# Optimization experiments

Measured on AMD Instinct MI355X. Metric: run time of the kernel, lower is better.

## Reference

```python
import jax, jax.numpy as jnp
import numpy as np

ALPHA = 0.2  # LeakyReLU negative slope


def _gat_layer(h, dst, adj, w, a_in, a_out, b):
    # h: [N, F_in], dst: [N, K] int (edge (i,k): i -> dst[i,k]), adj: [N, K]
    hid = h @ w                      # [N, D]
    s_in = hid @ a_in                # [N]  (attention applied to source-node half)
    s_out = hid @ a_out              # [N]  (attention applied to dest-node half)
    # edge scores, grouped per source node (matches view(-1, num_neighs) softmax)
    e = jax.nn.leaky_relu(s_in[:, None] + s_out[dst], ALPHA)   # [N, K]
    # torch code detaches attention (Variable(..., requires_grad=False))
    att = jax.lax.stop_gradient(jax.nn.softmax(e, axis=1))     # [N, K]
    w_edge = adj * att                                          # [N, K]
    # SpMM: out[i] = sum_k w_edge[i,k] * hid[dst[i,k]]
    out = jnp.einsum('nk,nkd->nd', w_edge, hid[dst]) + b        # [N, D]
    return out


def setup_inputs() -> dict:
    key = jax.random.key(0)
    ks = jax.random.split(key, 12)
    N, K, F, H, O = 100000, 16, 128, 128, 128
    stdv1 = 1.0 / np.sqrt(H)
    stdv2 = 1.0 / np.sqrt(O)
    u = lambda k, shp, s: jax.random.uniform(k, shp, jnp.float32, -s, s)
    return {
        'x': jax.random.normal(ks[0], (N, F), jnp.float32),
        'dst_idx': jax.random.randint(ks[1], (N, K), 0, N),
        'adj_vals': jax.random.uniform(ks[2], (N, K), jnp.float32),
        'w1': u(ks[3], (F, H), stdv1),
        'a_in1': jax.random.normal(ks[4], (H,), jnp.float32) * (1.414 / np.sqrt(H)),
        'a_out1': jax.random.normal(ks[5], (H,), jnp.float32) * (1.414 / np.sqrt(H)),
        'b1': u(ks[6], (H,), stdv1),
        'w2': u(ks[7], (H, O), stdv2),
        'a_in2': jax.random.normal(ks[8], (O,), jnp.float32) * (1.414 / np.sqrt(O)),
        'a_out2': jax.random.normal(ks[9], (O,), jnp.float32) * (1.414 / np.sqrt(O)),
        'b2': u(ks[10], (O,), stdv2),
    }


def reference(x, dst_idx, adj_vals, w1, a_in1, a_out1, b1, w2, a_in2, a_out2, b2):
    h = jax.nn.relu(_gat_layer(x, dst_idx, adj_vals, w1, a_in1, a_out1, b1))
    h = jax.nn.relu(_gat_layer(h, dst_idx, adj_vals, w2, a_in2, a_out2, b2))
    return h
```

## Files before the change

kernel.cpp:

```cpp
#include <hip/hip_runtime.h>

#define ALPHA 0.2f
#define LDA 136

typedef short bf16x8 __attribute__((ext_vector_type(8)));
typedef float f32x4  __attribute__((ext_vector_type(4)));

static __device__ __forceinline__ float bf2f(unsigned short u) {
    union { unsigned int i; float f; } v; v.i = ((unsigned int)u) << 16; return v.f;
}
static __device__ __forceinline__ unsigned short f2bf(float f) {
    union { float f; unsigned int i; } v; v.f = f;
    unsigned int x = v.i;
    return (unsigned short)((x + 0x7fffu + ((x >> 16) & 1u)) >> 16);
}

__global__ __launch_bounds__(128)
void prep_wT_kernel(const float* __restrict__ w1, const float* __restrict__ w2,
                    unsigned short* __restrict__ wT1, unsigned short* __restrict__ wT2)
{
    const int b = blockIdx.x;
    const float* w = (b >> 4) ? w2 : w1;
    unsigned short* wT = (b >> 4) ? wT2 : wT1;
    const int k0 = (b & 15) * 8;
    const int c = threadIdx.x;

    ushort4 u0, u1;
    u0.x = f2bf(w[(k0 + 0) * 128 + c]); u0.y = f2bf(w[(k0 + 1) * 128 + c]);
    u0.z = f2bf(w[(k0 + 2) * 128 + c]); u0.w = f2bf(w[(k0 + 3) * 128 + c]);
    u1.x = f2bf(w[(k0 + 4) * 128 + c]); u1.y = f2bf(w[(k0 + 5) * 128 + c]);
    u1.z = f2bf(w[(k0 + 6) * 128 + c]); u1.w = f2bf(w[(k0 + 7) * 128 + c]);
    *(ushort4*)&wT[c * 128 + k0]     = u0;
    *(ushort4*)&wT[c * 128 + k0 + 4] = u1;
}

template <bool SRC_BF>
__global__ __launch_bounds__(256)
void gemm_score_mfma(const void* __restrict__ srcv,
                     const unsigned short* __restrict__ wT,
                     const float* __restrict__ a_in,
                     const float* __restrict__ a_out,
                     unsigned short* __restrict__ hid,
                     float* __restrict__ s_in,
                     float* __restrict__ s_out,
                     int n)
{
    __shared__ short Es[64 * LDA];
    __shared__ float aS[2][128];

    const int tid  = threadIdx.x;
    const int lane = tid & 63;
    const int wv   = tid >> 6;
    const int m    = lane & 15;
    const int q    = lane >> 4;
    const int rbase = blockIdx.x * 64;
    const int row   = rbase + wv * 16 + m;
    const bool rok  = (row < n);

    if (tid < 128) { aS[0][tid] = a_in[tid]; aS[1][tid] = a_out[tid]; }
    __syncthreads();

    bf16x8 aF[4];
    if (SRC_BF) {
        const unsigned short* src = (const unsigned short*)srcv;
        const unsigned short* p = &src[(size_t)row * 128 + q * 8];
        #pragma unroll
        for (int ks = 0; ks < 4; ks++)
            aF[ks] = rok ? *(const bf16x8*)(p + ks * 32) : (bf16x8){0,0,0,0,0,0,0,0};
    } else {
        const float* src = (const float*)srcv;
        const float* p = &src[(size_t)row * 128 + q * 8];
        #pragma unroll
        for (int ks = 0; ks < 4; ks++) {
            if (rok) {
                float4 v0 = *(const float4*)(p + ks * 32);
                float4 v1 = *(const float4*)(p + ks * 32 + 4);
                bf16x8 a;
                a[0] = (short)f2bf(v0.x); a[1] = (short)f2bf(v0.y);
                a[2] = (short)f2bf(v0.z); a[3] = (short)f2bf(v0.w);
                a[4] = (short)f2bf(v1.x); a[5] = (short)f2bf(v1.y);
                a[6] = (short)f2bf(v1.z); a[7] = (short)f2bf(v1.w);
                aF[ks] = a;
            } else aF[ks] = (bf16x8){0,0,0,0,0,0,0,0};
        }
    }

    f32x4 acc[8];
    #pragma unroll
    for (int t = 0; t < 8; t++) acc[t] = (f32x4){0.f, 0.f, 0.f, 0.f};

    const unsigned short* Bp = &wT[m * 128 + q * 8];
    #pragma unroll
    for (int t = 0; t < 8; t++) {
        #pragma unroll
        for (int ks = 0; ks < 4; ks++) {
            bf16x8 bF = *(const bf16x8*)(Bp + ((size_t)t * 16 * 128) + ks * 32);
            acc[t] = __builtin_amdgcn_mfma_f32_16x16x32_bf16(aF[ks], bF, acc[t], 0, 0, 0);
        }
    }

    float pin[4] = {0.f, 0.f, 0.f, 0.f}, pout[4] = {0.f, 0.f, 0.f, 0.f};
    #pragma unroll
    for (int t = 0; t < 8; t++) {
        float ai = aS[0][t * 16 + m];
        float ao = aS[1][t * 16 + m];
        #pragma unroll
        for (int r = 0; r < 4; r++) {
            pin[r]  += acc[t][r] * ai;
            pout[r] += acc[t][r] * ao;
        }
    }
    #pragma unroll
    for (int msk = 8; msk >= 1; msk >>= 1) {
        #pragma unroll
        for (int r = 0; r < 4; r++) {
            pin[r]  += __shfl_xor(pin[r],  msk);
            pout[r] += __shfl_xor(pout[r], msk);
        }
    }
    if (m == 0) {
        #pragma unroll
        for (int r = 0; r < 4; r++) {
            int g = rbase + wv * 16 + q * 4 + r;
            if (g < n) { s_in[g] = pin[r]; s_out[g] = pout[r]; }
        }
    }

    #pragma unroll
    for (int t = 0; t < 8; t++)
        #pragma unroll
        for (int r = 0; r < 4; r++)
            Es[(wv * 16 + q * 4 + r) * LDA + t * 16 + m] = (short)f2bf(acc[t][r]);
    __syncthreads();
    #pragma unroll
    for (int i = 0; i < 4; i++) {
        int e = tid + i * 256;
        int r = e >> 4, j = (e & 15) * 8;
        int gr = rbase + r;
        if (gr < n) {
            int4 v = *(const int4*)&Es[r * LDA + j];
            *(int4*)&hid[(size_t)gr * 128 + j] = v;
        }
    }
}

template <bool FINAL>
__global__ __launch_bounds__(256)
void gat_aggregate_kernel(const unsigned short* __restrict__ hid,
                          const float* __restrict__ s_in,
                          const float* __restrict__ s_out,
                          const int* __restrict__ dst,
                          const float* __restrict__ adj,
                          const float* __restrict__ bias,
                          void* __restrict__ outv,
                          int n)
{
    const int lane = threadIdx.x & 63;
    const int node = (blockIdx.x * 256 + threadIdx.x) >> 6;
    if (node >= n) return;

    float sc = -1e30f;
    int dk = 0;
    float av = 0.f;
    if (lane < 16) {
        int ei = node * 16 + lane;
        dk = dst[ei];
        av = adj[ei];
        float e = s_in[node] + s_out[dk];
        sc = (e > 0.f) ? e : ALPHA * e;
    }
    float m = sc;
    #pragma unroll
    for (int msk = 8; msk >= 1; msk >>= 1) m = fmaxf(m, __shfl_xor(m, msk));
    float p = (lane < 16) ? __expf(sc - m) : 0.f;
    float s = p;
    #pragma unroll
    for (int msk = 8; msk >= 1; msk >>= 1) s += __shfl_xor(s, msk);
    float wk = (lane < 16) ? av * p / s : 0.f;

    const int sub = lane >> 4;
    const int oct = lane & 15;
    int   gdk[4];
    float gwk[4];
    #pragma unroll
    for (int j = 0; j < 4; j++) {
        gdk[j] = __shfl(dk, 4 * j + sub);
        gwk[j] = __shfl(wk, 4 * j + sub);
    }

    float acc[8];
    #pragma unroll
    for (int i = 0; i < 8; i++) acc[i] = 0.f;
    #pragma unroll
    for (int j = 0; j < 4; j++) {
        bf16x8 hv = *(const bf16x8*)&hid[(size_t)gdk[j] * 128 + oct * 8];
        float wj = gwk[j];
        #pragma unroll
        for (int i = 0; i < 8; i++)
            acc[i] += wj * bf2f((unsigned short)hv[i]);
    }
    #pragma unroll
    for (int i = 0; i < 8; i++) {
        acc[i] += __shfl_xor(acc[i], 16);
        acc[i] += __shfl_xor(acc[i], 32);
    }

    if (lane < 16) {
        float4 b0 = *(const float4*)&bias[oct * 8];
        float4 b1 = *(const float4*)&bias[oct * 8 + 4];
        float o[8];
        o[0] = fmaxf(acc[0] + b0.x, 0.f); o[1] = fmaxf(acc[1] + b0.y, 0.f);
        o[2] = fmaxf(acc[2] + b0.z, 0.f); o[3] = fmaxf(acc[3] + b0.w, 0.f);
        o[4] = fmaxf(acc[4] + b1.x, 0.f); o[5] = fmaxf(acc[5] + b1.y, 0.f);
        o[6] = fmaxf(acc[6] + b1.z, 0.f); o[7] = fmaxf(acc[7] + b1.w, 0.f);

        const size_t obase = (size_t)node * 128 + oct * 8;
        if (FINAL) {
            float* of = (float*)outv;
            *(float4*)&of[obase]     = make_float4(o[0], o[1], o[2], o[3]);
            *(float4*)&of[obase + 4] = make_float4(o[4], o[5], o[6], o[7]);
        } else {
            unsigned short* oh = (unsigned short*)outv;
            ushort4 u0, u1;
            u0.x = f2bf(o[0]); u0.y = f2bf(o[1]); u0.z = f2bf(o[2]); u0.w = f2bf(o[3]);
            u1.x = f2bf(o[4]); u1.y = f2bf(o[5]); u1.z = f2bf(o[6]); u1.w = f2bf(o[7]);
            *(ushort4*)&oh[obase]     = u0;
            *(ushort4*)&oh[obase + 4] = u1;
        }
    }
}

extern "C" void kernel_launch(void* const* d_in, const int* in_sizes, int n_in,
                              void* d_out, int out_size, void* d_ws, size_t ws_size,
                              hipStream_t stream)
{
    const float* x      = (const float*)d_in[0];
    const int*   dst    = (const int*)d_in[1];
    const float* adj    = (const float*)d_in[2];
    const float* w1     = (const float*)d_in[3];
    const float* a_in1  = (const float*)d_in[4];
    const float* a_out1 = (const float*)d_in[5];
    const float* b1     = (const float*)d_in[6];
    const float* w2     = (const float*)d_in[7];
    const float* a_in2  = (const float*)d_in[8];
    const float* a_out2 = (const float*)d_in[9];
    const float* b2     = (const float*)d_in[10];

    const int N = in_sizes[0] / 128;

    unsigned short* hid   = (unsigned short*)d_ws;
    float*          s_in  = (float*)(hid + (size_t)N * 128);
    float*          s_out = s_in + N;
    unsigned short* wT1   = (unsigned short*)(s_out + N);
    unsigned short* wT2   = wT1 + 128 * 128;
    unsigned short* h1    = (unsigned short*)d_out + out_size;

    dim3 blk(256);
    dim3 ggrid((N + 63) / 64);
    dim3 agrid((N + 3) / 4);

    prep_wT_kernel<<<32, 128, 0, stream>>>(w1, w2, wT1, wT2);

    gemm_score_mfma<false><<<ggrid, blk, 0, stream>>>(x,  wT1, a_in1, a_out1,
                                                      hid, s_in, s_out, N);
    gat_aggregate_kernel<false><<<agrid, blk, 0, stream>>>(hid, s_in, s_out, dst,
                                                           adj, b1, h1, N);
    gemm_score_mfma<true><<<ggrid, blk, 0, stream>>>(h1, wT2, a_in2, a_out2,
                                                     hid, s_in, s_out, N);
    gat_aggregate_kernel<true><<<agrid, blk, 0, stream>>>(hid, s_in, s_out, dst,
                                                          adj, b2, d_out, N);
}
```

Measured before the change: 304.7 us.

## Stage GEMM weights in LDS and restructure SpMM gather per-lane columns

New measurement: 259.3 us. -14.9%, faster.

```diff
diff --git a/kernel.cpp b/kernel.cpp
--- a/kernel.cpp
+++ b/kernel.cpp
@@ -35,7 +35,7 @@
 }
 
 template <bool SRC_BF>
-__global__ __launch_bounds__(256)
+__global__ __launch_bounds__(256, 4)
 void gemm_score_mfma(const void* __restrict__ srcv,
                      const unsigned short* __restrict__ wT,
                      const float* __restrict__ a_in,
@@ -45,7 +45,7 @@
                      float* __restrict__ s_out,
                      int n)
 {
-    __shared__ short Es[64 * LDA];
+    __shared__ short Bs[128 * LDA];
     __shared__ float aS[2][128];
 
     const int tid  = threadIdx.x;
@@ -58,7 +58,6 @@
     const bool rok  = (row < n);
 
     if (tid < 128) { aS[0][tid] = a_in[tid]; aS[1][tid] = a_out[tid]; }
-    __syncthreads();
 
     bf16x8 aF[4];
     if (SRC_BF) {
@@ -85,16 +84,25 @@
         }
     }
 
+    #pragma unroll
+    for (int i = 0; i < 8; i++) {
+        int e = tid + i * 256;
+        int nr = e >> 4, j = (e & 15) * 8;
+        int4 v = *(const int4*)&wT[nr * 128 + j];
+        *(int4*)&Bs[nr * LDA + j] = v;
+    }
+    __syncthreads();
+
     f32x4 acc[8];
     #pragma unroll
     for (int t = 0; t < 8; t++) acc[t] = (f32x4){0.f, 0.f, 0.f, 0.f};
 
-    const unsigned short* Bp = &wT[m * 128 + q * 8];
-    #pragma unroll
-    for (int t = 0; t < 8; t++) {
-        #pragma unroll
-        for (int ks = 0; ks < 4; ks++) {
-            bf16x8 bF = *(const bf16x8*)(Bp + ((size_t)t * 16 * 128) + ks * 32);
+    const short* Bbase = &Bs[m * LDA + q * 8];
+    #pragma unroll
+    for (int ks = 0; ks < 4; ks++) {
+        #pragma unroll
+        for (int t = 0; t < 8; t++) {
+            bf16x8 bF = *(const bf16x8*)(Bbase + t * 16 * LDA + ks * 32);
             acc[t] = __builtin_amdgcn_mfma_f32_16x16x32_bf16(aF[ks], bF, acc[t], 0, 0, 0);
         }
     }
@@ -126,6 +134,8 @@
         }
     }
 
+    __syncthreads();
+    short* Es = Bs;
     #pragma unroll
     for (int t = 0; t < 8; t++)
         #pragma unroll
@@ -178,55 +188,25 @@
     for (int msk = 8; msk >= 1; msk >>= 1) s += __shfl_xor(s, msk);
     float wk = (lane < 16) ? av * p / s : 0.f;
 
-    const int sub = lane >> 4;
-    const int oct = lane & 15;
-    int   gdk[4];
-    float gwk[4];
-    #pragma unroll
-    for (int j = 0; j < 4; j++) {
-        gdk[j] = __shfl(dk, 4 * j + sub);
-        gwk[j] = __shfl(wk, 4 * j + sub);
-    }
-
-    float acc[8];
-    #pragma unroll
-    for (int i = 0; i < 8; i++) acc[i] = 0.f;
-    #pragma unroll
-    for (int j = 0; j < 4; j++) {
-        bf16x8 hv = *(const bf16x8*)&hid[(size_t)gdk[j] * 128 + oct * 8];
-        float wj = gwk[j];
-        #pragma unroll
-        for (int i = 0; i < 8; i++)
-            acc[i] += wj * bf2f((unsigned short)hv[i]);
-    }
-    #pragma unroll
-    for (int i = 0; i < 8; i++) {
-        acc[i] += __shfl_xor(acc[i], 16);
-        acc[i] += __shfl_xor(acc[i], 32);
-    }
-
-    if (lane < 16) {
-        float4 b0 = *(const float4*)&bias[oct * 8];
-        float4 b1 = *(const float4*)&bias[oct * 8 + 4];
-        float o[8];
-        o[0] = fmaxf(acc[0] + b0.x, 0.f); o[1] = fmaxf(acc[1] + b0.y, 0.f);
-        o[2] = fmaxf(acc[2] + b0.z, 0.f); o[3] = fmaxf(acc[3] + b0.w, 0.f);
-        o[4] = fmaxf(acc[4] + b1.x, 0.f); o[5] = fmaxf(acc[5] + b1.y, 0.f);
-        o[6] = fmaxf(acc[6] + b1.z, 0.f); o[7] = fmaxf(acc[7] + b1.w, 0.f);
-
-        const size_t obase = (size_t)node * 128 + oct * 8;
-        if (FINAL) {
-            float* of = (float*)outv;
-            *(float4*)&of[obase]     = make_float4(o[0], o[1], o[2], o[3]);
-            *(float4*)&of[obase + 4] = make_float4(o[4], o[5], o[6], o[7]);
-        } else {
-            unsigned short* oh = (unsigned short*)outv;
-            ushort4 u0, u1;
-            u0.x = f2bf(o[0]); u0.y = f2bf(o[1]); u0.z = f2bf(o[2]); u0.w = f2bf(o[3]);
-            u1.x = f2bf(o[4]); u1.y = f2bf(o[5]); u1.z = f2bf(o[6]); u1.w = f2bf(o[7]);
-            *(ushort4*)&oh[obase]     = u0;
-            *(ushort4*)&oh[obase + 4] = u1;
-        }
+    const int c = lane * 2;
+    float accx = 0.f, accy = 0.f;
+    #pragma unroll
+    for (int k = 0; k < 16; k++) {
+        int   sdk = __builtin_amdgcn_readlane(dk, k);
+        float swk = __int_as_float(__builtin_amdgcn_readlane(__float_as_int(wk), k));
+        ushort2 hq = *(const ushort2*)&hid[(size_t)sdk * 128 + c];
+        accx += swk * bf2f(hq.x);
+        accy += swk * bf2f(hq.y);
+    }
+    float ox = fmaxf(accx + bias[c],     0.f);
+    float oy = fmaxf(accy + bias[c + 1], 0.f);
+
+    const size_t oidx = (size_t)node * 128 + c;
+    if (FINAL) {
+        *(float2*)&((float*)outv)[oidx] = make_float2(ox, oy);
+    } else {
+        ushort2 ov; ov.x = f2bf(ox); ov.y = f2bf(oy);
+        *(ushort2*)&((unsigned short*)outv)[oidx] = ov;
     }
 }
 
```
